# Performance work log

Measured on AMD Instinct MI355X. Metric: run time of the kernel, lower is better.

Reference implementation:

```python
import jax, jax.numpy as jnp
import numpy as np

NEG_SLOPE_GAT = 0.2   # PyG GATConv default negative_slope
NEG_SLOPE_ACT = 0.01  # torch F.leaky_relu default


def gat_conv(x, src, dst, W, att_src, att_dst, b, N):
    # Single-head PyG GATConv with self-loops already appended in (src, dst).
    xl = x @ W                              # [N, d]
    a_src = xl @ att_src                    # [N]
    a_dst = xl @ att_dst                    # [N]
    e = jax.nn.leaky_relu(a_src[src] + a_dst[dst], NEG_SLOPE_GAT)  # [E]
    m = jax.ops.segment_max(e, dst, num_segments=N)                # per-dst max
    ex = jnp.exp(e - m[dst])
    s = jax.ops.segment_sum(ex, dst, num_segments=N)
    alpha = ex / (s[dst] + 1e-16)                                  # softmax over in-edges
    out = jax.ops.segment_sum(alpha[:, None] * xl[src], dst, num_segments=N)
    return out + b


def setup_inputs() -> dict:
    key = jax.random.key(0)
    ks = jax.random.split(key, 10)
    N, E, d_in, h1, h2 = 100000, 1600000, 128, 128, 64
    x = jax.random.normal(ks[0], (N, d_in), dtype=jnp.float32)
    edge_index = jax.random.randint(ks[1], (2, E), 0, N, dtype=jnp.int64)
    s1 = 1.0 / np.sqrt(d_in)
    s2 = 1.0 / np.sqrt(h1)
    W1 = jax.random.uniform(ks[2], (d_in, h1), jnp.float32, -s1, s1)
    att_src1 = jax.random.uniform(ks[3], (h1,), jnp.float32, -s2, s2)
    att_dst1 = jax.random.uniform(ks[4], (h1,), jnp.float32, -s2, s2)
    b1 = jnp.zeros((h1,), jnp.float32)
    s3 = 1.0 / np.sqrt(h2)
    W2 = jax.random.uniform(ks[5], (h1, h2), jnp.float32, -s2, s2)
    att_src2 = jax.random.uniform(ks[6], (h2,), jnp.float32, -s3, s3)
    att_dst2 = jax.random.uniform(ks[7], (h2,), jnp.float32, -s3, s3)
    b2 = jnp.zeros((h2,), jnp.float32)
    return {"x": x, "edge_index": edge_index, "W1": W1, "att_src1": att_src1,
            "att_dst1": att_dst1, "b1": b1, "W2": W2, "att_src2": att_src2,
            "att_dst2": att_dst2, "b2": b2}


def reference(x, edge_index, W1, att_src1, att_dst1, b1, W2, att_src2, att_dst2, b2):
    N = x.shape[0]
    loops = jnp.arange(N, dtype=edge_index.dtype)
    src = jnp.concatenate([edge_index[0], loops])  # add self-loops (PyG default)
    dst = jnp.concatenate([edge_index[1], loops])
    h = gat_conv(x, src, dst, W1, att_src1, att_dst1, b1, N)
    h = jax.nn.leaky_relu(h, NEG_SLOPE_ACT)
    # dropout omitted (deterministic reference / eval mode)
    h = gat_conv(h, src, dst, W2, att_src2, att_dst2, b2, N)
    return jax.nn.softmax(h, axis=0)
```

## Files before the change

kernel.cpp:

```cpp
#include <hip/hip_runtime.h>
#include <hip/hip_fp16.h>
#include <math.h>


constexpr int NPARTS = 256;
constexpr int PCAP = 8192;
constexpr int CHUNK = 4096;
constexpr int DPPMAX = 400;

typedef _Float16 f16x8 __attribute__((ext_vector_type(8)));
typedef float f32x4 __attribute__((ext_vector_type(4)));

__device__ __forceinline__ int bcasti(int v, int j) {
  return __builtin_amdgcn_readlane(v, j);
}
__device__ __forceinline__ float bcastf(float v, int j) {
  return __uint_as_float((unsigned)__builtin_amdgcn_readlane((int)__float_as_uint(v), j));
}
__device__ __forceinline__ __half2 xor32h(__half2 v) {
  int i = *(int*)&v;
  i = __shfl_xor(i, 32);
  return *(__half2*)&i;
}

__global__ __launch_bounds__(256) void k_build1(
    const int* __restrict__ srcA, const int* __restrict__ dstA,
    int* __restrict__ pcur, uint2* __restrict__ parts,
    int* __restrict__ ovf, int* __restrict__ ovf_cnt,
    const float* __restrict__ W1, const float* __restrict__ W2,
    _Float16* __restrict__ Wf1, _Float16* __restrict__ Wf2,
    int E, int N, int DPP, int nch, int ovfcap) {
  if ((int)blockIdx.x >= nch) {
    int t = ((int)blockIdx.x - nch) * 256 + (int)threadIdx.x;
    const int stride = 8 * 256;
    for (int i = t; i < 8 * 4 * 64 * 8; i += stride) {
      int j = i & 7, l = (i >> 3) & 63, kk = (i >> 9) & 3, cb = i >> 11;
      int k = kk * 32 + (l >> 4) * 8 + j, c = cb * 16 + (l & 15);
      Wf1[i] = (_Float16)W1[k * 128 + c];
    }
    for (int i = t; i < 4 * 4 * 64 * 8; i += stride) {
      int j = i & 7, l = (i >> 3) & 63, kk = (i >> 9) & 3, cb = i >> 11;
      int k = kk * 32 + (l >> 4) * 8 + j, c = cb * 16 + (l & 15);
      Wf2[i] = (_Float16)W2[k * 64 + c];
    }
    return;
  }
  __shared__ int hist[NPARTS];
  __shared__ int base[NPARTS];
  const int tot = E + N;
  const int c = blockIdx.x;
  hist[threadIdx.x] = 0;
  __syncthreads();
  const int beg = c * CHUNK;
  int pp[16], rr[16], ss[16], dd[16];
#pragma unroll
  for (int j = 0; j < 16; ++j) {
    int e = beg + j * 256 + (int)threadIdx.x;
    int d = -1, s = 0;
    if (e < tot) {
      if (e < E) { d = dstA[e]; s = srcA[e]; } else { d = s = e - E; }
    }
    dd[j] = d; ss[j] = s;
    int p = (d >= 0) ? (d / DPP) : -1;
    pp[j] = p;
    rr[j] = (p >= 0) ? atomicAdd(&hist[p], 1) : 0;
  }
  __syncthreads();
  base[threadIdx.x] = atomicAdd(&pcur[threadIdx.x], hist[threadIdx.x]);
  __syncthreads();
#pragma unroll
  for (int j = 0; j < 16; ++j) {
    int p = pp[j];
    if (p < 0) continue;
    int pos = base[p] + rr[j];
    if (pos < PCAP) {
      parts[(size_t)p * PCAP + pos] = make_uint2((unsigned)ss[j], (unsigned)dd[j]);
    } else {
      int o = atomicAdd(ovf_cnt, 1);
      if (o < ovfcap) { ovf[2 * o] = dd[j]; ovf[2 * o + 1] = ss[j]; }
    }
  }
}

template <int C, typename XT>
__device__ __forceinline__ void gemm_mfma_body(
    const XT* __restrict__ X, const _Float16* __restrict__ Wf,
    const float* __restrict__ atts, const float* __restrict__ attd,
    __half* __restrict__ XLh, float* __restrict__ a_s, float* __restrict__ a_d,
    int N, int bid) {
  constexpr int NCB = C / 16;
  const int lane = threadIdx.x & 63;
  const int wv = threadIdx.x >> 6;
  const int r0 = bid * 64 + wv * 16;
  const int arow = lane & 15;
  const int grp = lane >> 4;
  const int r = r0 + arow;
  const int rsafe = (r < N) ? r : (N - 1);

  float av[NCB], dv[NCB];
#pragma unroll
  for (int cb = 0; cb < NCB; ++cb) {
    av[cb] = atts[cb * 16 + arow];
    dv[cb] = attd[cb * 16 + arow];
  }

  f16x8 af[4];
  if constexpr (sizeof(XT) == 4) {
    const float* xr = (const float*)X + (size_t)rsafe * 128 + grp * 8;
#pragma unroll
    for (int kk = 0; kk < 4; ++kk) {
      float4 u0 = *(const float4*)(xr + kk * 32);
      float4 u1 = *(const float4*)(xr + kk * 32 + 4);
      af[kk][0] = (_Float16)u0.x; af[kk][1] = (_Float16)u0.y;
      af[kk][2] = (_Float16)u0.z; af[kk][3] = (_Float16)u0.w;
      af[kk][4] = (_Float16)u1.x; af[kk][5] = (_Float16)u1.y;
      af[kk][6] = (_Float16)u1.z; af[kk][7] = (_Float16)u1.w;
    }
  } else {
    const __half* xr = (const __half*)X + (size_t)rsafe * 128 + grp * 8;
#pragma unroll
    for (int kk = 0; kk < 4; ++kk)
      af[kk] = *(const f16x8*)(xr + kk * 32);
  }

  float ps[4] = {0.f, 0.f, 0.f, 0.f};
  float pd[4] = {0.f, 0.f, 0.f, 0.f};

#pragma unroll
  for (int cb = 0; cb < NCB; ++cb) {
    f32x4 acc = {0.f, 0.f, 0.f, 0.f};
#pragma unroll
    for (int kk = 0; kk < 4; ++kk) {
      f16x8 bf = *(const f16x8*)(Wf + ((size_t)(cb * 4 + kk) * 64 + lane) * 8);
      acc = __builtin_amdgcn_mfma_f32_16x16x32_f16(af[kk], bf, acc, 0, 0, 0);
    }
    const int ocol = cb * 16 + arow;
#pragma unroll
    for (int i = 0; i < 4; ++i) {
      const int orow = r0 + grp * 4 + i;
      if (orow < N) XLh[(size_t)orow * C + ocol] = (__half)(_Float16)acc[i];
      ps[i] = fmaf(acc[i], av[cb], ps[i]);
      pd[i] = fmaf(acc[i], dv[cb], pd[i]);
    }
  }
#pragma unroll
  for (int m = 1; m < 16; m <<= 1) {
#pragma unroll
    for (int i = 0; i < 4; ++i) {
      ps[i] += __shfl_xor(ps[i], m);
      pd[i] += __shfl_xor(pd[i], m);
    }
  }
  if (arow == 0) {
#pragma unroll
    for (int i = 0; i < 4; ++i) {
      const int orow = r0 + grp * 4 + i;
      if (orow < N) { a_s[orow] = ps[i]; a_d[orow] = pd[i]; }
    }
  }
}

struct PlaceSmem {
  int sc[NPARTS];
  int l_cnt[DPPMAX];
  int l_off[DPPMAX];
  int l_out[PCAP];
};

__global__ __launch_bounds__(256) void k_gemm1_place(
    const float* __restrict__ X, const _Float16* __restrict__ Wf,
    const float* __restrict__ atts, const float* __restrict__ attd,
    __half* __restrict__ XLh, float* __restrict__ a_s, float* __restrict__ a_d,
    int N, const uint2* __restrict__ parts, const int* __restrict__ pcur,
    int* __restrict__ rowptr, int* __restrict__ seidx,
    int DPP, int nparts, int gb) {
  __shared__ PlaceSmem sm;
  if ((int)blockIdx.x < gb) {
    gemm_mfma_body<128, float>(X, Wf, atts, attd, XLh, a_s, a_d, N, blockIdx.x);
    return;
  }
  const int p = (int)blockIdx.x - gb;
  const int t = threadIdx.x;
  sm.sc[t] = min(pcur[t], PCAP);
  __syncthreads();
  for (int o = 1; o < NPARTS; o <<= 1) {
    int x = (t >= o) ? sm.sc[t - o] : 0;
    __syncthreads();
    sm.sc[t] += x;
    __syncthreads();
  }
  const int base = (p == 0) ? 0 : sm.sc[p - 1];
  const int n = sm.sc[p] - base;
  const int d0 = p * DPP;
  const int ndst = min(DPP, N - d0);
  const uint2* pe = parts + (size_t)p * PCAP;

  for (int i = t; i < ndst; i += 256) sm.l_cnt[i] = 0;
  __syncthreads();
  for (int i = t; i < n; i += 256) {
    uint2 e = pe[i];
    atomicAdd(&sm.l_cnt[(int)e.y - d0], 1);
  }
  __syncthreads();
  if (t == 0) {
    int run = 0;
    for (int i = 0; i < ndst; ++i) { sm.l_off[i] = run; run += sm.l_cnt[i]; }
  }
  __syncthreads();
  for (int i = t; i < ndst; i += 256) {
    rowptr[d0 + i] = base + sm.l_off[i];
    sm.l_cnt[i] = sm.l_off[i];
  }
  if (p == nparts - 1 && t == 0) rowptr[N] = sm.sc[nparts - 1];
  __syncthreads();
  for (int i = t; i < n; i += 256) {
    uint2 e = pe[i];
    int pos = atomicAdd(&sm.l_cnt[(int)e.y - d0], 1);
    sm.l_out[pos] = (int)e.x;
  }
  __syncthreads();
  for (int i = t; i < n; i += 256)
    seidx[base + i] = sm.l_out[i];
}

__global__ __launch_bounds__(256) void k_gemm_l2(
    const __half* __restrict__ X, const _Float16* __restrict__ Wf,
    const float* __restrict__ atts, const float* __restrict__ attd,
    __half* __restrict__ XLh, float* __restrict__ a_s, float* __restrict__ a_d,
    int N) {
  gemm_mfma_body<64, __half>(X, Wf, atts, attd, XLh, a_s, a_d, N, blockIdx.x);
}

__global__ __launch_bounds__(256) void k_aggr_l1(
    const __half* __restrict__ XLh, const float* __restrict__ as_,
    const float* __restrict__ ad_, const int* __restrict__ rowptr,
    const int* __restrict__ seidx, const int* __restrict__ ovf,
    const int* __restrict__ ovf_cnt, const float* __restrict__ bias,
    __half* __restrict__ OUT, int N) {
  constexpr int C = 128;
  const int lane = threadIdx.x & 63;
  const int wid = threadIdx.x >> 6;
  const int grp = lane >> 5;
  const int l5 = lane & 31;
  const int novf = *ovf_cnt;
  float bb[4];
#pragma unroll
  for (int j = 0; j < 4; ++j) bb[j] = bias[4 * l5 + j];

  for (int d = blockIdx.x * 4 + wid; d < N; d += gridDim.x * 4) {
    const int beg = rowptr[d], end = rowptr[d + 1];
    const int nb = end - beg;
    const float adst = ad_[d];

    float s;
    int sv = 0; float ev = 0.f;
    if (nb <= 64) {
      if (lane < nb) {
        sv = seidx[beg + lane];
        float t = as_[sv] + adst;
        t = t > 0.f ? t : 0.2f * t;
        ev = __expf(t);
      }
      s = ev;
    } else {
      s = 0.f;
      for (int i = beg + lane; i < end; i += 64) {
        int s2 = seidx[i];
        float t = as_[s2] + adst;
        t = t > 0.f ? t : 0.2f * t;
        s += __expf(t);
      }
    }
#pragma unroll
    for (int o = 32; o; o >>= 1) s += __shfl_xor(s, o);

    if (novf > 0) {
      float so = 0.f;
      for (int i = lane; i < novf; i += 64) {
        if (ovf[2 * i] == d) {
          float t = as_[ovf[2 * i + 1]] + adst;
          t = t > 0.f ? t : 0.2f * t;
          so += __expf(t);
        }
      }
#pragma unroll
      for (int o = 32; o; o >>= 1) so += __shfl_xor(so, o);
      s += so;
    }
    const float inv = 1.f / (s + 1e-16f);

    __half2 ac01 = __floats2half2_rn(0.f, 0.f);
    __half2 ac23 = __floats2half2_rn(0.f, 0.f);
    auto pair = [&](int vsrc, float vw, int j, int cnt) {
      const int j0 = 2 * j, j1 = 2 * j + 1;
      const int s0 = bcasti(vsrc, j0);
      const float w0 = bcastf(vw, j0);
      int s1 = s0; float w1 = 0.f;
      if (j1 < cnt) { s1 = bcasti(vsrc, j1); w1 = bcastf(vw, j1); }
      const int sb = grp ? s1 : s0;
      const float wj = grp ? w1 : w0;
      const unsigned off = ((unsigned)sb << 8) + ((unsigned)l5 << 3);
      const uint2 raw = *(const uint2*)((const char*)XLh + off);
      const __half2 wh = __float2half2_rn(wj);
      ac01 = __hfma2(wh, *(const __half2*)&raw.x, ac01);
      ac23 = __hfma2(wh, *(const __half2*)&raw.y, ac23);
    };

    if (nb <= 64) {
      const float wv = ev * inv;
      const int np = (nb + 1) >> 1;
      int j = 0;
      for (; j + 4 <= np; j += 4) {
        pair(sv, wv, j, nb); pair(sv, wv, j + 1, nb);
        pair(sv, wv, j + 2, nb); pair(sv, wv, j + 3, nb);
      }
      for (; j < np; ++j) pair(sv, wv, j, nb);
    } else {
      for (int i0 = beg; i0 < end; i0 += 64) {
        const int nc = min(64, end - i0);
        int sc = 0; float wc = 0.f;
        if (lane < nc) {
          sc = seidx[i0 + lane];
          float t = as_[sc] + adst;
          t = t > 0.f ? t : 0.2f * t;
          wc = __expf(t) * inv;
        }
        const int np = (nc + 1) >> 1;
        for (int j = 0; j < np; ++j) pair(sc, wc, j, nc);
      }
    }

    ac01 = __hadd2(ac01, xor32h(ac01));
    ac23 = __hadd2(ac23, xor32h(ac23));
    float2 f01 = __half22float2(ac01);
    float2 f23 = __half22float2(ac23);
    float a0 = f01.x, a1 = f01.y, a2 = f23.x, a3 = f23.y;

    if (novf > 0) {
      for (int i = 0; i < novf; ++i) {
        if (ovf[2 * i] != d) continue;
        int os = ovf[2 * i + 1];
        float t = as_[os] + adst;
        t = t > 0.f ? t : 0.2f * t;
        float wj = __expf(t) * inv;
        const float2 raw = *(const float2*)(XLh + (size_t)os * C + l5 * 4);
        float2 x0 = __half22float2(*(const __half2*)&raw.x);
        float2 x1 = __half22float2(*(const __half2*)&raw.y);
        a0 = fmaf(wj, x0.x, a0);
        a1 = fmaf(wj, x0.y, a1);
        a2 = fmaf(wj, x1.x, a2);
        a3 = fmaf(wj, x1.y, a3);
      }
    }

    if (grp == 0) {
      float o0 = a0 + bb[0], o1 = a1 + bb[1];
      float o2 = a2 + bb[2], o3 = a3 + bb[3];
      o0 = o0 > 0.f ? o0 : 0.01f * o0;
      o1 = o1 > 0.f ? o1 : 0.01f * o1;
      o2 = o2 > 0.f ? o2 : 0.01f * o2;
      o3 = o3 > 0.f ? o3 : 0.01f * o3;
      __half2 p0 = __floats2half2_rn(o0, o1);
      __half2 p1 = __floats2half2_rn(o2, o3);
      uint2 u;
      u.x = *(unsigned*)&p0;
      u.y = *(unsigned*)&p1;
      *(uint2*)(OUT + (size_t)d * C + l5 * 4) = u;
    }
  }
}

__global__ __launch_bounds__(256) void k_aggr2(
    const __half* __restrict__ XLh, const float* __restrict__ as_,
    const float* __restrict__ ad_, const int* __restrict__ rowptr,
    const int* __restrict__ seidx, const int* __restrict__ ovf,
    const int* __restrict__ ovf_cnt, const float* __restrict__ bias,
    float* __restrict__ OUT, float* __restrict__ csum8, int N) {
  constexpr int C = 64;
  const int lane = threadIdx.x & 63;
  const int wid = threadIdx.x >> 6;
  const int grp = lane >> 5;
  const int l5 = lane & 31;
  const int novf = *ovf_cnt;
  const float bb0 = bias[2 * l5], bb1 = bias[2 * l5 + 1];
  float cs0 = 0.f, cs1 = 0.f;

  for (int d = blockIdx.x * 4 + wid; d < N; d += gridDim.x * 4) {
    const int beg = rowptr[d], end = rowptr[d + 1];
    const int nb = end - beg;
    const float adst = ad_[d];

    float s;
    int sv = 0; float ev = 0.f;
    if (nb <= 64) {
      if (lane < nb) {
        sv = seidx[beg + lane];
        float t = as_[sv] + adst;
        t = t > 0.f ? t : 0.2f * t;
        ev = __expf(t);
      }
      s = ev;
    } else {
      s = 0.f;
      for (int i = beg + lane; i < end; i += 64) {
        int s2 = seidx[i];
        float t = as_[s2] + adst;
        t = t > 0.f ? t : 0.2f * t;
        s += __expf(t);
      }
    }
#pragma unroll
    for (int o = 32; o; o >>= 1) s += __shfl_xor(s, o);

    if (novf > 0) {
      float so = 0.f;
      for (int i = lane; i < novf; i += 64) {
        if (ovf[2 * i] == d) {
          float t = as_[ovf[2 * i + 1]] + adst;
          t = t > 0.f ? t : 0.2f * t;
          so += __expf(t);
        }
      }
#pragma unroll
      for (int o = 32; o; o >>= 1) so += __shfl_xor(so, o);
      s += so;
    }
    const float inv = 1.f / (s + 1e-16f);

    __half2 ac = __floats2half2_rn(0.f, 0.f);
    auto pair = [&](int vsrc, float vw, int j, int cnt) {
      const int j0 = 2 * j, j1 = 2 * j + 1;
      const int s0 = bcasti(vsrc, j0);
      const float w0 = bcastf(vw, j0);
      int s1 = s0; float w1 = 0.f;
      if (j1 < cnt) { s1 = bcasti(vsrc, j1); w1 = bcastf(vw, j1); }
      const int sb = grp ? s1 : s0;
      const float wj = grp ? w1 : w0;
      const unsigned off = ((unsigned)sb << 7) + ((unsigned)l5 << 2);
      const __half2 hv = *(const __half2*)((const char*)XLh + off);
      ac = __hfma2(__float2half2_rn(wj), hv, ac);
    };

    if (nb <= 64) {
      const float wv = ev * inv;
      const int np = (nb + 1) >> 1;
      int j = 0;
      for (; j + 4 <= np; j += 4) {
        pair(sv, wv, j, nb); pair(sv, wv, j + 1, nb);
        pair(sv, wv, j + 2, nb); pair(sv, wv, j + 3, nb);
      }
      for (; j < np; ++j) pair(sv, wv, j, nb);
    } else {
      for (int i0 = beg; i0 < end; i0 += 64) {
        const int nc = min(64, end - i0);
        int sc = 0; float wc = 0.f;
        if (lane < nc) {
          sc = seidx[i0 + lane];
          float t = as_[sc] + adst;
          t = t > 0.f ? t : 0.2f * t;
          wc = __expf(t) * inv;
        }
        const int np = (nc + 1) >> 1;
        for (int j = 0; j < np; ++j) pair(sc, wc, j, nc);
      }
    }

    ac = __hadd2(ac, xor32h(ac));
    float2 fa = __half22float2(ac);
    float a0 = fa.x, a1 = fa.y;

    if (novf > 0) {
      for (int i = 0; i < novf; ++i) {
        if (ovf[2 * i] != d) continue;
        int os = ovf[2 * i + 1];
        float t = as_[os] + adst;
        t = t > 0.f ? t : 0.2f * t;
        float wj = __expf(t) * inv;
        const __half2 hv = *(const __half2*)(XLh + (size_t)os * C + l5 * 2);
        float2 xv = __half22float2(hv);
        a0 = fmaf(wj, xv.x, a0);
        a1 = fmaf(wj, xv.y, a1);
      }
    }

    if (grp == 0) {
      float o0 = a0 + bb0;
      float o1 = a1 + bb1;
      *(float2*)&OUT[(size_t)d * C + 2 * l5] = make_float2(o0, o1);
      cs0 += __expf(o0);
      cs1 += __expf(o1);
    }
  }

  __shared__ float csA[4][64];
  if (grp == 0) { csA[wid][2 * l5] = cs0; csA[wid][2 * l5 + 1] = cs1; }
  __syncthreads();
  if (threadIdx.x < 64) {
    float tot = csA[0][threadIdx.x] + csA[1][threadIdx.x] +
                csA[2][threadIdx.x] + csA[3][threadIdx.x];
    if (tot != 0.f)
      atomicAdd(&csum8[((int)blockIdx.x & 7) * 64 + (int)threadIdx.x], tot);
  }
}

__global__ void k_norm(float* __restrict__ O, const float* __restrict__ csum8,
                       size_t tot4) {
  __shared__ float cs[64];
  if (threadIdx.x < 64) {
    float s = 0.f;
#pragma unroll
    for (int r = 0; r < 8; ++r) s += csum8[r * 64 + (int)threadIdx.x];
    cs[threadIdx.x] = s;
  }
  __syncthreads();
  for (size_t i = blockIdx.x * (size_t)blockDim.x + threadIdx.x; i < tot4;
       i += (size_t)gridDim.x * blockDim.x) {
    float4 v = ((float4*)O)[i];
    int c0 = (int)((i * 4) & 63);
    v.x = __expf(v.x) / cs[c0];
    v.y = __expf(v.y) / cs[c0 + 1];
    v.z = __expf(v.z) / cs[c0 + 2];
    v.w = __expf(v.w) / cs[c0 + 3];
    ((float4*)O)[i] = v;
  }
}

extern "C" void kernel_launch(void* const* d_in, const int* in_sizes, int n_in,
                              void* d_out, int out_size, void* d_ws, size_t ws_size,
                              hipStream_t stream) {
  const float* x   = (const float*)d_in[0];
  const int*   ei  = (const int*)d_in[1];
  const float* W1  = (const float*)d_in[2];
  const float* as1 = (const float*)d_in[3];
  const float* ad1 = (const float*)d_in[4];
  const float* b1  = (const float*)d_in[5];
  const float* W2  = (const float*)d_in[6];
  const float* as2 = (const float*)d_in[7];
  const float* ad2 = (const float*)d_in[8];
  const float* b2  = (const float*)d_in[9];
  float* out = (float*)d_out;

  const int N = in_sizes[0] / 128;
  const int E = in_sizes[1] / 2;
  const int Etot = E + N;
  const int* srcA = ei;
  const int* dstA = ei + E;
  const int DPP = (N + NPARTS - 1) / NPARTS;
  const int nparts = (N + DPP - 1) / DPP;

  char* w = (char*)d_ws;
  auto take = [&](size_t bytes) -> void* {
    void* p = (void*)w;
    w += (bytes + 255) & ~(size_t)255;
    return p;
  };
  __half*    xlh   = (__half*)take((size_t)N * 128 * 2);
  __half*    xl2h  = (__half*)take((size_t)N * 64 * 2);
  __half*    h     = (__half*)take((size_t)N * 128 * 2);
  float*     a_s   = (float*)take((size_t)N * 4);
  float*     a_d   = (float*)take((size_t)N * 4);
  int*       zeroB = (int*)take((size_t)(1 + NPARTS + 512) * 4);
  int*       ovf_cnt = zeroB;
  int*       pcur    = zeroB + 1;
  float*     csum8   = (float*)(zeroB + 1 + NPARTS);
  int*       rowptr = (int*)take((size_t)(N + 1) * 4);
  int*       seidx  = (int*)take((size_t)Etot * 4);
  int*       ovf    = (int*)take((size_t)Etot * 2 * 4);
  uint2*     parts  = (uint2*)take((size_t)NPARTS * PCAP * 8);
  _Float16*  wf1    = (_Float16*)take((size_t)8 * 4 * 64 * 8 * 2);
  _Float16*  wf2    = (_Float16*)take((size_t)4 * 4 * 64 * 8 * 2);

  hipMemsetAsync(zeroB, 0, (size_t)(1 + NPARTS + 512) * 4, stream);

  const int nch = (Etot + CHUNK - 1) / CHUNK;
  const int gb = (N + 63) / 64;

  k_build1<<<nch + 8, 256, 0, stream>>>(srcA, dstA, pcur, parts, ovf, ovf_cnt,
                                        W1, W2, wf1, wf2, E, N, DPP, nch, Etot);
  k_gemm1_place<<<gb + NPARTS, 256, 0, stream>>>(
      x, wf1, as1, ad1, xlh, a_s, a_d, N, parts, pcur, rowptr, seidx,
      DPP, nparts, gb);
  k_aggr_l1<<<8192, 256, 0, stream>>>(xlh, a_s, a_d, rowptr, seidx, ovf, ovf_cnt,
                                      b1, h, N);
  k_gemm_l2<<<gb, 256, 0, stream>>>(h, wf2, as2, ad2, xl2h, a_s, a_d, N);
  k_aggr2<<<8192, 256, 0, stream>>>(xl2h, a_s, a_d, rowptr, seidx, ovf, ovf_cnt,
                                    b2, out, csum8, N);
  const size_t tot4 = (size_t)N * 64 / 4;
  k_norm<<<2048, 256, 0, stream>>>(out, csum8, tot4);
}
```

Baseline: 222.0 us.

## Pack partition edges into 32-bit words and widen layer-2 aggregation to four edges

Partition buckets now store each edge as a single 32-bit word, with the local destination offset in the high bits and the source index in the low 17 bits, instead of an 8-byte pair. This halves the bucket traffic written by the build kernel and read twice by the placement kernel. Separately, the layer-2 aggregation now handles four edges per step, with 16 lanes each loading 8 bytes (4 halves), in place of two edges with 32 lanes loading 4 bytes. It then reduces with two xor shuffles and writes float4 outputs. The packing assumes source indices fit in 17 bits, which holds for N=100000 but caps the supported graph size.

```diff
diff --git a/kernel.cpp b/kernel.cpp
--- a/kernel.cpp
+++ b/kernel.cpp
@@ -7,6 +7,7 @@
 constexpr int PCAP = 8192;
 constexpr int CHUNK = 4096;
 constexpr int DPPMAX = 400;
+constexpr int SRCB = 17;
 
 typedef _Float16 f16x8 __attribute__((ext_vector_type(8)));
 typedef float f32x4 __attribute__((ext_vector_type(4)));
@@ -17,15 +18,15 @@
 __device__ __forceinline__ float bcastf(float v, int j) {
   return __uint_as_float((unsigned)__builtin_amdgcn_readlane((int)__float_as_uint(v), j));
 }
-__device__ __forceinline__ __half2 xor32h(__half2 v) {
+__device__ __forceinline__ __half2 xorh(__half2 v, int m) {
   int i = *(int*)&v;
-  i = __shfl_xor(i, 32);
+  i = __shfl_xor(i, m);
   return *(__half2*)&i;
 }
 
 __global__ __launch_bounds__(256) void k_build1(
     const int* __restrict__ srcA, const int* __restrict__ dstA,
-    int* __restrict__ pcur, uint2* __restrict__ parts,
+    int* __restrict__ pcur, unsigned* __restrict__ parts,
     int* __restrict__ ovf, int* __restrict__ ovf_cnt,
     const float* __restrict__ W1, const float* __restrict__ W2,
     _Float16* __restrict__ Wf1, _Float16* __restrict__ Wf2,
@@ -52,7 +53,9 @@
   hist[threadIdx.x] = 0;
   __syncthreads();
   const int beg = c * CHUNK;
-  int pp[16], rr[16], ss[16], dd[16];
+  int pp[16], rr[16];
+  unsigned pk[16];
+  int dd[16], ss[16];
 #pragma unroll
   for (int j = 0; j < 16; ++j) {
     int e = beg + j * 256 + (int)threadIdx.x;
@@ -60,9 +63,10 @@
     if (e < tot) {
       if (e < E) { d = dstA[e]; s = srcA[e]; } else { d = s = e - E; }
     }
-    dd[j] = d; ss[j] = s;
     int p = (d >= 0) ? (d / DPP) : -1;
     pp[j] = p;
+    dd[j] = d; ss[j] = s;
+    pk[j] = (p >= 0) ? (((unsigned)(d - p * DPP) << SRCB) | (unsigned)s) : 0u;
     rr[j] = (p >= 0) ? atomicAdd(&hist[p], 1) : 0;
   }
   __syncthreads();
@@ -74,7 +78,7 @@
     if (p < 0) continue;
     int pos = base[p] + rr[j];
     if (pos < PCAP) {
-      parts[(size_t)p * PCAP + pos] = make_uint2((unsigned)ss[j], (unsigned)dd[j]);
+      parts[(size_t)p * PCAP + pos] = pk[j];
     } else {
       int o = atomicAdd(ovf_cnt, 1);
       if (o < ovfcap) { ovf[2 * o] = dd[j]; ovf[2 * o + 1] = ss[j]; }
@@ -171,7 +175,7 @@
     const float* __restrict__ X, const _Float16* __restrict__ Wf,
     const float* __restrict__ atts, const float* __restrict__ attd,
     __half* __restrict__ XLh, float* __restrict__ a_s, float* __restrict__ a_d,
-    int N, const uint2* __restrict__ parts, const int* __restrict__ pcur,
+    int N, const unsigned* __restrict__ parts, const int* __restrict__ pcur,
     int* __restrict__ rowptr, int* __restrict__ seidx,
     int DPP, int nparts, int gb) {
   __shared__ PlaceSmem sm;
@@ -193,13 +197,13 @@
   const int n = sm.sc[p] - base;
   const int d0 = p * DPP;
   const int ndst = min(DPP, N - d0);
-  const uint2* pe = parts + (size_t)p * PCAP;
+  const unsigned* pe = parts + (size_t)p * PCAP;
 
   for (int i = t; i < ndst; i += 256) sm.l_cnt[i] = 0;
   __syncthreads();
   for (int i = t; i < n; i += 256) {
-    uint2 e = pe[i];
-    atomicAdd(&sm.l_cnt[(int)e.y - d0], 1);
+    unsigned e = pe[i];
+    atomicAdd(&sm.l_cnt[e >> SRCB], 1);
   }
   __syncthreads();
   if (t == 0) {
@@ -214,9 +218,9 @@
   if (p == nparts - 1 && t == 0) rowptr[N] = sm.sc[nparts - 1];
   __syncthreads();
   for (int i = t; i < n; i += 256) {
-    uint2 e = pe[i];
-    int pos = atomicAdd(&sm.l_cnt[(int)e.y - d0], 1);
-    sm.l_out[pos] = (int)e.x;
+    unsigned e = pe[i];
+    int pos = atomicAdd(&sm.l_cnt[e >> SRCB], 1);
+    sm.l_out[pos] = (int)(e & ((1u << SRCB) - 1u));
   }
   __syncthreads();
   for (int i = t; i < n; i += 256)
@@ -330,8 +334,8 @@
       }
     }
 
-    ac01 = __hadd2(ac01, xor32h(ac01));
-    ac23 = __hadd2(ac23, xor32h(ac23));
+    ac01 = __hadd2(ac01, xorh(ac01, 32));
+    ac23 = __hadd2(ac23, xorh(ac23, 32));
     float2 f01 = __half22float2(ac01);
     float2 f23 = __half22float2(ac23);
     float a0 = f01.x, a1 = f01.y, a2 = f23.x, a3 = f23.y;
@@ -379,11 +383,13 @@
   constexpr int C = 64;
   const int lane = threadIdx.x & 63;
   const int wid = threadIdx.x >> 6;
-  const int grp = lane >> 5;
-  const int l5 = lane & 31;
+  const int q = lane >> 4;
+  const int li = lane & 15;
   const int novf = *ovf_cnt;
-  const float bb0 = bias[2 * l5], bb1 = bias[2 * l5 + 1];
-  float cs0 = 0.f, cs1 = 0.f;
+  float bb[4];
+#pragma unroll
+  for (int j = 0; j < 4; ++j) bb[j] = bias[4 * li + j];
+  float cs0 = 0.f, cs1 = 0.f, cs2 = 0.f, cs3 = 0.f;
 
   for (int d = blockIdx.x * 4 + wid; d < N; d += gridDim.x * 4) {
     const int beg = rowptr[d], end = rowptr[d + 1];
@@ -427,29 +433,39 @@
     }
     const float inv = 1.f / (s + 1e-16f);
 
-    __half2 ac = __floats2half2_rn(0.f, 0.f);
-    auto pair = [&](int vsrc, float vw, int j, int cnt) {
-      const int j0 = 2 * j, j1 = 2 * j + 1;
+    __half2 ac01 = __floats2half2_rn(0.f, 0.f);
+    __half2 ac23 = __floats2half2_rn(0.f, 0.f);
+    auto quad = [&](int vsrc, float vw, int j, int cnt) {
+      const int j0 = 4 * j;
       const int s0 = bcasti(vsrc, j0);
       const float w0 = bcastf(vw, j0);
-      int s1 = s0; float w1 = 0.f;
-      if (j1 < cnt) { s1 = bcasti(vsrc, j1); w1 = bcastf(vw, j1); }
-      const int sb = grp ? s1 : s0;
-      const float wj = grp ? w1 : w0;
-      const unsigned off = ((unsigned)sb << 7) + ((unsigned)l5 << 2);
-      const __half2 hv = *(const __half2*)((const char*)XLh + off);
-      ac = __hfma2(__float2half2_rn(wj), hv, ac);
+      int s1 = s0, s2 = s0, s3 = s0;
+      float w1 = 0.f, w2 = 0.f, w3 = 0.f;
+      if (j0 + 1 < cnt) { s1 = bcasti(vsrc, j0 + 1); w1 = bcastf(vw, j0 + 1); }
+      if (j0 + 2 < cnt) { s2 = bcasti(vsrc, j0 + 2); w2 = bcastf(vw, j0 + 2); }
+      if (j0 + 3 < cnt) { s3 = bcasti(vsrc, j0 + 3); w3 = bcastf(vw, j0 + 3); }
+      const int sA = (q & 1) ? s1 : s0;
+      const int sB = (q & 1) ? s3 : s2;
+      const int sb = (q & 2) ? sB : sA;
+      const float wA = (q & 1) ? w1 : w0;
+      const float wB = (q & 1) ? w3 : w2;
+      const float wj = (q & 2) ? wB : wA;
+      const unsigned off = ((unsigned)sb << 7) + ((unsigned)li << 3);
+      const uint2 raw = *(const uint2*)((const char*)XLh + off);
+      const __half2 wh = __float2half2_rn(wj);
+      ac01 = __hfma2(wh, *(const __half2*)&raw.x, ac01);
+      ac23 = __hfma2(wh, *(const __half2*)&raw.y, ac23);
     };
 
     if (nb <= 64) {
       const float wv = ev * inv;
-      const int np = (nb + 1) >> 1;
+      const int np = (nb + 3) >> 2;
       int j = 0;
       for (; j + 4 <= np; j += 4) {
-        pair(sv, wv, j, nb); pair(sv, wv, j + 1, nb);
-        pair(sv, wv, j + 2, nb); pair(sv, wv, j + 3, nb);
-      }
-      for (; j < np; ++j) pair(sv, wv, j, nb);
+        quad(sv, wv, j, nb); quad(sv, wv, j + 1, nb);
+        quad(sv, wv, j + 2, nb); quad(sv, wv, j + 3, nb);
+      }
+      for (; j < np; ++j) quad(sv, wv, j, nb);
     } else {
       for (int i0 = beg; i0 < end; i0 += 64) {
         const int nc = min(64, end - i0);
@@ -460,14 +476,18 @@
           t = t > 0.f ? t : 0.2f * t;
           wc = __expf(t) * inv;
         }
-        const int np = (nc + 1) >> 1;
-        for (int j = 0; j < np; ++j) pair(sc, wc, j, nc);
-      }
-    }
-
-    ac = __hadd2(ac, xor32h(ac));
-    float2 fa = __half22float2(ac);
-    float a0 = fa.x, a1 = fa.y;
+        const int np = (nc + 3) >> 2;
+        for (int j = 0; j < np; ++j) quad(sc, wc, j, nc);
+      }
+    }
+
+    ac01 = __hadd2(ac01, xorh(ac01, 16));
+    ac01 = __hadd2(ac01, xorh(ac01, 32));
+    ac23 = __hadd2(ac23, xorh(ac23, 16));
+    ac23 = __hadd2(ac23, xorh(ac23, 32));
+    float2 f01 = __half22float2(ac01);
+    float2 f23 = __half22float2(ac23);
+    float a0 = f01.x, a1 = f01.y, a2 = f23.x, a3 = f23.y;
 
     if (novf > 0) {
       for (int i = 0; i < novf; ++i) {
@@ -476,24 +496,35 @@
         float t = as_[os] + adst;
         t = t > 0.f ? t : 0.2f * t;
         float wj = __expf(t) * inv;
-        const __half2 hv = *(const __half2*)(XLh + (size_t)os * C + l5 * 2);
-        float2 xv = __half22float2(hv);
-        a0 = fmaf(wj, xv.x, a0);
-        a1 = fmaf(wj, xv.y, a1);
-      }
-    }
-
-    if (grp == 0) {
-      float o0 = a0 + bb0;
-      float o1 = a1 + bb1;
-      *(float2*)&OUT[(size_t)d * C + 2 * l5] = make_float2(o0, o1);
+        const float2 raw = *(const float2*)(XLh + (size_t)os * C + li * 4);
+        float2 x0 = __half22float2(*(const __half2*)&raw.x);
+        float2 x1 = __half22float2(*(const __half2*)&raw.y);
+        a0 = fmaf(wj, x0.x, a0);
+        a1 = fmaf(wj, x0.y, a1);
+        a2 = fmaf(wj, x1.x, a2);
+        a3 = fmaf(wj, x1.y, a3);
+      }
+    }
+
+    if (q == 0) {
+      float o0 = a0 + bb[0], o1 = a1 + bb[1];
+      float o2 = a2 + bb[2], o3 = a3 + bb[3];
+      float4 ov = make_float4(o0, o1, o2, o3);
+      *(float4*)&OUT[(size_t)d * C + 4 * li] = ov;
       cs0 += __expf(o0);
       cs1 += __expf(o1);
+      cs2 += __expf(o2);
+      cs3 += __expf(o3);
     }
   }
 
   __shared__ float csA[4][64];
-  if (grp == 0) { csA[wid][2 * l5] = cs0; csA[wid][2 * l5 + 1] = cs1; }
+  if (q == 0) {
+    csA[wid][4 * li + 0] = cs0;
+    csA[wid][4 * li + 1] = cs1;
+    csA[wid][4 * li + 2] = cs2;
+    csA[wid][4 * li + 3] = cs3;
+  }
   __syncthreads();
   if (threadIdx.x < 64) {
     float tot = csA[0][threadIdx.x] + csA[1][threadIdx.x] +
@@ -566,7 +597,7 @@
   int*       rowptr = (int*)take((size_t)(N + 1) * 4);
   int*       seidx  = (int*)take((size_t)Etot * 4);
   int*       ovf    = (int*)take((size_t)Etot * 2 * 4);
-  uint2*     parts  = (uint2*)take((size_t)NPARTS * PCAP * 8);
+  unsigned*  parts  = (unsigned*)take((size_t)NPARTS * PCAP * 4);
   _Float16*  wf1    = (_Float16*)take((size_t)8 * 4 * 64 * 8 * 2);
   _Float16*  wf2    = (_Float16*)take((size_t)4 * 4 * 64 * 8 * 2);
 
```

Measured after the change: 218.4 us. Within noise of the previous version (-1.6%).
